# Optimization experiments

Measured on AMD Instinct MI355X. Metric: run time of the kernel, lower is better.

Reference implementation:

```python
import jax, jax.numpy as jnp
import numpy as np

T = 3
B, N, F = 8, 256, 32
E_DIM = 8
HID = 32
IN_DIM = 2 * (F + 1) + E_DIM  # 74


def setup_inputs() -> dict:
    key = jax.random.key(0)
    ks = jax.random.split(key, 10)
    h = jax.random.normal(ks[0], (B, N, F), dtype=jnp.float32)
    e = jax.random.uniform(ks[1], (B, N, N, E_DIM), dtype=jnp.float32)
    q = jax.random.normal(ks[2], (B, N, 1), dtype=jnp.float32)
    mask = jnp.ones((B, N), dtype=jnp.float32)
    s1 = 1.0 / np.sqrt(IN_DIM)
    s2 = 1.0 / np.sqrt(HID)
    W1 = jax.random.normal(ks[3], (T, IN_DIM, HID), dtype=jnp.float32) * s1
    b1 = jnp.zeros((T, HID), dtype=jnp.float32)
    W2 = jax.random.normal(ks[4], (T, HID, HID), dtype=jnp.float32) * s2
    b2 = jnp.zeros((T, HID), dtype=jnp.float32)
    W3 = jax.random.normal(ks[5], (T, HID, 1), dtype=jnp.float32) * s2
    b3 = jnp.zeros((T, 1), dtype=jnp.float32)
    return {"h": h, "e": e, "q": q, "mask": mask,
            "W1": W1, "b1": b1, "W2": W2, "b2": b2, "W3": W3, "b3": b3}


def reference(h, e, q, mask, W1, b1, W2, b2, W3, b3):
    tol = jnp.float32(1e-8)
    clip = jnp.clip(e, tol, 1e5)
    largest_e = jnp.max(clip, axis=-1)          # [B,N,N]
    is_near = (largest_e != tol).astype(h.dtype)
    m = mask.astype(h.dtype)
    exp_mask = m[:, :, None] * m[:, None, :]    # [B,N,N]
    natom = e.shape[1]

    def mlp(x, t):
        x = jax.nn.relu(jnp.matmul(x, W1[t]) + b1[t])
        x = jax.nn.relu(jnp.matmul(x, W2[t]) + b2[t])
        return (jnp.matmul(x, W3[t]) + b3[t])[..., 0]  # [B,N,N]

    for t in range(T):
        inp = jnp.concatenate([h, q], axis=-1)  # [B,N,F+1]
        d = inp.shape[-1]
        inp_i = jnp.broadcast_to(inp[:, :, None, :], (inp.shape[0], natom, natom, d))
        inp_j = jnp.broadcast_to(inp[:, None, :, :], (inp.shape[0], natom, natom, d))
        inp_ij = jnp.concatenate([inp_i, inp_j, e], axis=-1)  # [B,N,N,IN_DIM]
        inp_ji = jnp.concatenate([inp_j, inp_i, e], axis=-1)
        elec_ij = mlp(inp_ij, t)
        elec_ji = mlp(inp_ji, t)
        antisym = 0.5 * (elec_ij - elec_ji) * exp_mask * is_near
        q = q + jnp.sum(antisym, axis=2)[..., None]
    return q
```

## Files before the change

### kernel.cpp

```cpp
#include <hip/hip_runtime.h>
#include <hip/hip_bf16.h>


typedef __attribute__((ext_vector_type(8))) short short8;
typedef __attribute__((ext_vector_type(4))) float f32x4;
union U4S8 { uint4 u; short8 s; };
#define F4(p) (*(const float4*)(p))

__device__ __forceinline__ unsigned pkbf2(float lo, float hi) {
    unsigned a = __bfloat16_as_ushort(__float2bfloat16(lo));
    unsigned b = __bfloat16_as_ushort(__float2bfloat16(hi));
    return a | (b << 16);
}
__device__ __forceinline__ float bf2f(unsigned short u) {
    return __uint_as_float(((unsigned)u) << 16);
}

__global__ __launch_bounds__(256) void epn_pre(
    const float* __restrict__ h, const float* __restrict__ W1,
    const float* __restrict__ b1, const float* __restrict__ W2,
    unsigned short* __restrict__ basePbf, unsigned short* __restrict__ baseQbf,
    unsigned* __restrict__ W2T, uint4* __restrict__ WA)
{
    const int t  = blockIdx.x >> 8;
    const int lg = (blockIdx.x & 255) * 256 + threadIdx.x;
    const float* W1t = W1 + t*74*32;
    if (lg < 512) {
        int n = lg >> 4, kp = lg & 15;
        const float* W2t = W2 + t*1024;
        W2T[t*512 + lg] = pkbf2(W2t[(2*kp)*32 + n], W2t[(2*kp+1)*32 + n]);
    } else if (lg < 640) {
        int g2 = lg - 512;
        int kt = g2 >> 6, lane = g2 & 63;
        int l15 = lane & 15, sl = lane >> 4;
        float v[8];
        #pragma unroll
        for (int p = 0; p < 8; ++p) {
            int d = sl*8 + p;
            v[p] = (d < 8) ? W1t[(66+d)*32 + kt*16 + l15]
                           : ((kt*16 + l15 == d - 8) ? 1.0f : 0.0f);
        }
        WA[t*128 + g2] = make_uint4(pkbf2(v[0],v[1]), pkbf2(v[2],v[3]),
                                    pkbf2(v[4],v[5]), pkbf2(v[6],v[7]));
    }
    const int node = lg >> 5, k = lg & 31;
    const float* hn = h + node*32;
    float p = b1[t*32 + k], qq = 0.f;
    #pragma unroll
    for (int f = 0; f < 32; ++f) {
        float hv = hn[f];
        p  += hv * W1t[f*32 + k];
        qq += hv * W1t[(33+f)*32 + k];
    }
    basePbf[t*65536 + lg] = __bfloat16_as_ushort(__float2bfloat16(p));
    baseQbf[t*65536 + lg] = __bfloat16_as_ushort(__float2bfloat16(qq));
}

__global__ __launch_bounds__(256, 4) void epn_main(
    const float* __restrict__ e, const float* __restrict__ mask,
    const uint4* __restrict__ bP4, const uint4* __restrict__ bQ4,
    const float* __restrict__ qrowP, const float* __restrict__ qrowQ,
    const uint4* __restrict__ W2T4, const uint4* __restrict__ WA,
    const float* __restrict__ b2, const float* __restrict__ W3,
    const float* __restrict__ q_src, float* __restrict__ q_dst)
{
    __shared__ uint4 sx[9][256];
    __shared__ float red[4];

    const int bi = blockIdx.x, b = bi >> 8;
    const int tid = threadIdx.x, j = tid;
    const int lane = tid & 63, w = tid >> 6;
    const int l15 = lane & 15, sl = lane >> 4;

    float qj = q_src[b*256 + j];
    unsigned qpk = __bfloat16_as_ushort(__float2bfloat16(qj));
    const float* ejp = e + ((size_t)bi*256 + j)*8;
    float4 e0 = F4(ejp), e1 = F4(ejp + 4);
    float mx = fmaxf(fmaxf(fmaxf(e0.x,e0.y),fmaxf(e0.z,e0.w)),
                     fmaxf(fmaxf(e1.x,e1.y),fmaxf(e1.z,e1.w)));
    float nearf = (fminf(fmaxf(mx, 1e-8f), 1e5f) != 1e-8f) ? 1.f : 0.f;
    float mn = mask[bi] * mask[b*256 + j] * nearf;
    sx[0][j] = make_uint4(pkbf2(e0.x,e0.y), pkbf2(e0.z,e0.w),
                          pkbf2(e1.x,e1.y), pkbf2(e1.z,e1.w));
    {
        const uint4* bq = bQ4 + (size_t)(b*256 + j)*4;
        const uint4* bp = bP4 + (size_t)(b*256 + j)*4;
        sx[1][j]=bq[0]; sx[2][j]=bq[1]; sx[3][j]=bq[2]; sx[4][j]=bq[3];
        sx[5][j]=bp[0]; sx[6][j]=bp[1]; sx[7][j]=bp[2]; sx[8][j]=bp[3];
    }

    U4S8 wa00, wa01, wa1;
    wa00.u = WA[lane];
    wa01.u = WA[64 + lane];
    wa1.u  = make_uint4(0u,0u,0u,0u);
    if (sl == 0 && l15 >= 8) {
        int p = l15 - 8;
        unsigned v = 0x3F80u << ((p & 1) * 16);
        wa1.u.x = ((p>>1)==0)?v:0u;  wa1.u.y = ((p>>1)==1)?v:0u;
        wa1.u.z = ((p>>1)==2)?v:0u;  wa1.u.w = ((p>>1)==3)?v:0u;
    }
    unsigned aqQ0 = 0, aqQ1 = 0, aqP0 = 0, aqP1 = 0;
    if (sl == 0) {
        aqQ0 = __bfloat16_as_ushort(__float2bfloat16(qrowQ[l15]));
        aqQ1 = __bfloat16_as_ushort(__float2bfloat16(qrowQ[16 + l15]));
        aqP0 = __bfloat16_as_ushort(__float2bfloat16(qrowP[l15]));
        aqP1 = __bfloat16_as_ushort(__float2bfloat16(qrowP[16 + l15]));
    }
    float qi = q_src[bi];
    const unsigned short* bPi = (const unsigned short*)bP4 + (size_t)bi*32;
    const unsigned short* bQi = (const unsigned short*)bQ4 + (size_t)bi*32;
    f32x4 ckP0, ckP1, ckQ0, ckQ1;
    #pragma unroll
    for (int r = 0; r < 4; ++r) {
        int k0 = sl*4 + r, k1 = 16 + sl*4 + r;
        ckP0[r] = bf2f(bPi[k0]) + qi * qrowP[k0];
        ckP1[r] = bf2f(bPi[k1]) + qi * qrowP[k1];
        ckQ0[r] = bf2f(bQi[k0]) + qi * qrowQ[k0];
        ckQ1[r] = bf2f(bQi[k1]) + qi * qrowQ[k1];
    }
    U4S8 bu0, bu1;
    bu0.u = W2T4[l15*4 + sl];
    bu1.u = W2T4[(l15 + 16)*4 + sl];
    float b2v0 = b2[l15], b2v1 = b2[l15+16];
    float w3v0 = W3[l15], w3v1 = W3[l15+16];
    const int srcA = ((sl & 1) << 5) + l15, srcB = srcA + 16;
    const bool ktHi = (sl >= 2);
    const int slot0_d0 = (sl == 0) ? 0 : sl;
    const int slot0_d1 = (sl == 0) ? 0 : 4 + sl;

    float tot = 0.f;
    #pragma unroll
    for (int rt = 0; rt < 4; ++rt) {
        const int rl  = rt*16 + l15;
        const int row = w*64 + rl;
        unsigned qr = __shfl(qpk, rl);
        U4S8 bc2; bc2.u = make_uint4((sl == 0) ? (qr & 0xFFFFu) : 0u, 0u, 0u, 0u);
        float pA[4], pB[4];
        #pragma unroll
        for (int dir = 0; dir < 2; ++dir) {
            U4S8 bc0, bc1, aq0, aq1;
            bc0.u = sx[dir ? slot0_d1 : slot0_d0][row];
            bc1.u = sx[dir ? 8 : 4][row];
            aq0.u = make_uint4(dir ? aqP0 : aqQ0, 0u, 0u, 0u);
            aq1.u = make_uint4(dir ? aqP1 : aqQ1, 0u, 0u, 0u);
            f32x4 c0 = dir ? ckQ0 : ckP0;
            f32x4 c1 = dir ? ckQ1 : ckP1;
            f32x4 dk0 = __builtin_amdgcn_mfma_f32_16x16x32_bf16(wa00.s, bc0.s, c0, 0,0,0);
            dk0 = __builtin_amdgcn_mfma_f32_16x16x32_bf16(aq0.s, bc2.s, dk0, 0,0,0);
            f32x4 dk1 = __builtin_amdgcn_mfma_f32_16x16x32_bf16(wa01.s, bc0.s, c1, 0,0,0);
            dk1 = __builtin_amdgcn_mfma_f32_16x16x32_bf16(wa1.s,  bc1.s, dk1, 0,0,0);
            dk1 = __builtin_amdgcn_mfma_f32_16x16x32_bf16(aq1.s,  bc2.s, dk1, 0,0,0);
            unsigned pk00 = pkbf2(fmaxf(dk0[0],0.f), fmaxf(dk0[1],0.f));
            unsigned pk01 = pkbf2(fmaxf(dk0[2],0.f), fmaxf(dk0[3],0.f));
            unsigned pk10 = pkbf2(fmaxf(dk1[0],0.f), fmaxf(dk1[1],0.f));
            unsigned pk11 = pkbf2(fmaxf(dk1[2],0.f), fmaxf(dk1[3],0.f));
            unsigned sA0l = __shfl(pk00, srcA), sA0h = __shfl(pk10, srcA);
            unsigned sA1l = __shfl(pk01, srcA), sA1h = __shfl(pk11, srcA);
            unsigned sB0l = __shfl(pk00, srcB), sB0h = __shfl(pk10, srcB);
            unsigned sB1l = __shfl(pk01, srcB), sB1h = __shfl(pk11, srcB);
            U4S8 a;
            a.u.x = ktHi ? sA0h : sA0l;
            a.u.y = ktHi ? sA1h : sA1l;
            a.u.z = ktHi ? sB0h : sB0l;
            a.u.w = ktHi ? sB1h : sB1l;
            f32x4 z = {0.f, 0.f, 0.f, 0.f};
            f32x4 d0 = __builtin_amdgcn_mfma_f32_16x16x32_bf16(a.s, bu0.s, z, 0,0,0);
            f32x4 d1 = __builtin_amdgcn_mfma_f32_16x16x32_bf16(a.s, bu1.s, z, 0,0,0);
            float* pp = dir ? pB : pA;
            pp[0] = fmaxf(d0[0]+b2v0,0.f)*w3v0 + fmaxf(d1[0]+b2v1,0.f)*w3v1;
            pp[1] = fmaxf(d0[1]+b2v0,0.f)*w3v0 + fmaxf(d1[1]+b2v1,0.f)*w3v1;
            pp[2] = fmaxf(d0[2]+b2v0,0.f)*w3v0 + fmaxf(d1[2]+b2v1,0.f)*w3v1;
            pp[3] = fmaxf(d0[3]+b2v0,0.f)*w3v0 + fmaxf(d1[3]+b2v1,0.f)*w3v1;
        }
        const int jb = rt*16 + sl*4;
        float m0 = __shfl(mn, jb+0), m1 = __shfl(mn, jb+1);
        float m2 = __shfl(mn, jb+2), m3 = __shfl(mn, jb+3);
        tot += m0*(pA[0]-pB[0]) + m1*(pA[1]-pB[1])
             + m2*(pA[2]-pB[2]) + m3*(pA[3]-pB[3]);
    }
    #pragma unroll
    for (int off = 32; off > 0; off >>= 1) tot += __shfl_down(tot, off);
    if (lane == 0) red[w] = tot;
    __syncthreads();
    if (tid == 0)
        q_dst[bi] = q_src[bi] + 0.5f * (red[0] + red[1] + red[2] + red[3]);
}

extern "C" void kernel_launch(void* const* d_in, const int* in_sizes, int n_in,
                              void* d_out, int out_size, void* d_ws, size_t ws_size,
                              hipStream_t stream) {
    (void)in_sizes; (void)n_in; (void)out_size; (void)ws_size;
    const float* h    = (const float*)d_in[0];
    const float* e    = (const float*)d_in[1];
    const float* q    = (const float*)d_in[2];
    const float* mask = (const float*)d_in[3];
    const float* W1   = (const float*)d_in[4];
    const float* b1   = (const float*)d_in[5];
    const float* W2   = (const float*)d_in[6];
    const float* b2   = (const float*)d_in[7];
    const float* W3   = (const float*)d_in[8];

    char* ws = (char*)d_ws;
    unsigned short* basePbf = (unsigned short*)ws;
    unsigned short* baseQbf = (unsigned short*)(ws + 393216);
    float*    qA  = (float*)(ws + 786432);
    float*    qB  = (float*)(ws + 794624);
    unsigned* W2T = (unsigned*)(ws + 802816);
    uint4*    WA  = (uint4*)(ws + 808960);

    epn_pre<<<768, 256, 0, stream>>>(h, W1, b1, W2, basePbf, baseQbf, W2T, WA);

    const float* qsrc = q;
    for (int t = 0; t < 3; ++t) {
        float* qdst = (t == 2) ? (float*)d_out : (t == 0 ? qA : qB);
        epn_main<<<2048, 256, 0, stream>>>(
            e, mask,
            (const uint4*)(basePbf + t*65536), (const uint4*)(baseQbf + t*65536),
            W1 + t*74*32 + 32*32, W1 + t*74*32 + 65*32,
            (const uint4*)(W2T + t*512), WA + t*128,
            b2 + t*32, W3 + t*32, qsrc, qdst);
        qsrc = qdst;
    }
}
```

Baseline: 58.10 us.

## Fuse pre-pass and three timesteps into one persistent kernel with grid barriers

```diff
diff --git a/kernel.cpp b/kernel.cpp
--- a/kernel.cpp
+++ b/kernel.cpp
@@ -16,174 +16,234 @@
     return __uint_as_float(((unsigned)u) << 16);
 }
 
-__global__ __launch_bounds__(256) void epn_pre(
-    const float* __restrict__ h, const float* __restrict__ W1,
-    const float* __restrict__ b1, const float* __restrict__ W2,
+__device__ __forceinline__ void gbar(unsigned* bar, unsigned target) {
+    __syncthreads();
+    if (threadIdx.x == 0) {
+        __threadfence();
+        atomicAdd(bar, 1u);
+        while (__hip_atomic_load(bar, __ATOMIC_ACQUIRE,
+                                 __HIP_MEMORY_SCOPE_AGENT) < target)
+            __builtin_amdgcn_s_sleep(2);
+        __threadfence();
+    }
+    __syncthreads();
+}
+
+__global__ __launch_bounds__(256, 2) void epn_fused(
+    const float* __restrict__ h, const float* __restrict__ e,
+    const float* __restrict__ q0, const float* __restrict__ mask,
+    const float* __restrict__ W1, const float* __restrict__ b1,
+    const float* __restrict__ W2, const float* __restrict__ b2,
+    const float* __restrict__ W3,
     unsigned short* __restrict__ basePbf, unsigned short* __restrict__ baseQbf,
-    unsigned* __restrict__ W2T, uint4* __restrict__ WA)
+    unsigned* __restrict__ W2T, uint4* __restrict__ WA,
+    float* __restrict__ qA, float* __restrict__ qB, float* __restrict__ qOut,
+    unsigned* __restrict__ bar)
 {
-    const int t  = blockIdx.x >> 8;
-    const int lg = (blockIdx.x & 255) * 256 + threadIdx.x;
-    const float* W1t = W1 + t*74*32;
-    if (lg < 512) {
-        int n = lg >> 4, kp = lg & 15;
-        const float* W2t = W2 + t*1024;
-        W2T[t*512 + lg] = pkbf2(W2t[(2*kp)*32 + n], W2t[(2*kp+1)*32 + n]);
-    } else if (lg < 640) {
-        int g2 = lg - 512;
-        int kt = g2 >> 6, lane = g2 & 63;
-        int l15 = lane & 15, sl = lane >> 4;
-        float v[8];
-        #pragma unroll
-        for (int p = 0; p < 8; ++p) {
-            int d = sl*8 + p;
-            v[p] = (d < 8) ? W1t[(66+d)*32 + kt*16 + l15]
-                           : ((kt*16 + l15 == d - 8) ? 1.0f : 0.0f);
-        }
-        WA[t*128 + g2] = make_uint4(pkbf2(v[0],v[1]), pkbf2(v[2],v[3]),
-                                    pkbf2(v[4],v[5]), pkbf2(v[6],v[7]));
-    }
-    const int node = lg >> 5, k = lg & 31;
-    const float* hn = h + node*32;
-    float p = b1[t*32 + k], qq = 0.f;
-    #pragma unroll
-    for (int f = 0; f < 32; ++f) {
-        float hv = hn[f];
-        p  += hv * W1t[f*32 + k];
-        qq += hv * W1t[(33+f)*32 + k];
-    }
-    basePbf[t*65536 + lg] = __bfloat16_as_ushort(__float2bfloat16(p));
-    baseQbf[t*65536 + lg] = __bfloat16_as_ushort(__float2bfloat16(qq));
-}
-
-__global__ __launch_bounds__(256, 4) void epn_main(
-    const float* __restrict__ e, const float* __restrict__ mask,
-    const uint4* __restrict__ bP4, const uint4* __restrict__ bQ4,
-    const float* __restrict__ qrowP, const float* __restrict__ qrowQ,
-    const uint4* __restrict__ W2T4, const uint4* __restrict__ WA,
-    const float* __restrict__ b2, const float* __restrict__ W3,
-    const float* __restrict__ q_src, float* __restrict__ q_dst)
-{
-    __shared__ uint4 sx[9][256];
-    __shared__ float red[4];
-
-    const int bi = blockIdx.x, b = bi >> 8;
-    const int tid = threadIdx.x, j = tid;
+    __shared__ uint4 sxJ[8][256];
+    __shared__ uint4 se[2][256];
+    __shared__ float red[16];
+
+    const int tid  = threadIdx.x, j = tid;
     const int lane = tid & 63, w = tid >> 6;
-    const int l15 = lane & 15, sl = lane >> 4;
-
-    float qj = q_src[b*256 + j];
-    unsigned qpk = __bfloat16_as_ushort(__float2bfloat16(qj));
-    const float* ejp = e + ((size_t)bi*256 + j)*8;
-    float4 e0 = F4(ejp), e1 = F4(ejp + 4);
-    float mx = fmaxf(fmaxf(fmaxf(e0.x,e0.y),fmaxf(e0.z,e0.w)),
-                     fmaxf(fmaxf(e1.x,e1.y),fmaxf(e1.z,e1.w)));
-    float nearf = (fminf(fmaxf(mx, 1e-8f), 1e5f) != 1e-8f) ? 1.f : 0.f;
-    float mn = mask[bi] * mask[b*256 + j] * nearf;
-    sx[0][j] = make_uint4(pkbf2(e0.x,e0.y), pkbf2(e0.z,e0.w),
-                          pkbf2(e1.x,e1.y), pkbf2(e1.z,e1.w));
-    {
-        const uint4* bq = bQ4 + (size_t)(b*256 + j)*4;
-        const uint4* bp = bP4 + (size_t)(b*256 + j)*4;
-        sx[1][j]=bq[0]; sx[2][j]=bq[1]; sx[3][j]=bq[2]; sx[4][j]=bq[3];
-        sx[5][j]=bp[0]; sx[6][j]=bp[1]; sx[7][j]=bp[2]; sx[8][j]=bp[3];
-    }
-
-    U4S8 wa00, wa01, wa1;
-    wa00.u = WA[lane];
-    wa01.u = WA[64 + lane];
-    wa1.u  = make_uint4(0u,0u,0u,0u);
+    const int l15  = lane & 15, sl = lane >> 4;
+    const int bi0  = blockIdx.x * 4;
+    const int b    = bi0 >> 8;
+
+    for (int g = blockIdx.x * 256 + tid; g < 198528; g += 131072) {
+        if (g < 196608) {
+            int t = g >> 16, lg = g & 65535;
+            const float* W1t = W1 + t*2368;
+            int node = lg >> 5, k = lg & 31;
+            const float* hn = h + node*32;
+            float p = b1[t*32 + k], qq = 0.f;
+            #pragma unroll
+            for (int f = 0; f < 32; ++f) {
+                float hv = hn[f];
+                p  += hv * W1t[f*32 + k];
+                qq += hv * W1t[(33+f)*32 + k];
+            }
+            basePbf[g] = __bfloat16_as_ushort(__float2bfloat16(p));
+            baseQbf[g] = __bfloat16_as_ushort(__float2bfloat16(qq));
+        } else if (g < 198144) {
+            int gg = g - 196608;
+            int t = gg >> 9, lg = gg & 511;
+            int n = lg >> 4, kp = lg & 15;
+            const float* W2t = W2 + t*1024;
+            W2T[gg] = pkbf2(W2t[(2*kp)*32 + n], W2t[(2*kp+1)*32 + n]);
+        } else {
+            int gg = g - 198144;
+            int t = gg >> 7, g2 = gg & 127;
+            int kt = g2 >> 6, ln = g2 & 63;
+            int L15 = ln & 15, SL = ln >> 4;
+            const float* W1t = W1 + t*2368;
+            float v[8];
+            #pragma unroll
+            for (int p2 = 0; p2 < 8; ++p2) {
+                int d = SL*8 + p2;
+                v[p2] = (d < 8) ? W1t[(66+d)*32 + kt*16 + L15]
+                                : ((kt*16 + L15 == d - 8) ? 1.0f : 0.0f);
+            }
+            WA[gg] = make_uint4(pkbf2(v[0],v[1]), pkbf2(v[2],v[3]),
+                                pkbf2(v[4],v[5]), pkbf2(v[6],v[7]));
+        }
+    }
+
+    U4S8 wa1; wa1.u = make_uint4(0u,0u,0u,0u);
     if (sl == 0 && l15 >= 8) {
         int p = l15 - 8;
         unsigned v = 0x3F80u << ((p & 1) * 16);
         wa1.u.x = ((p>>1)==0)?v:0u;  wa1.u.y = ((p>>1)==1)?v:0u;
         wa1.u.z = ((p>>1)==2)?v:0u;  wa1.u.w = ((p>>1)==3)?v:0u;
     }
-    unsigned aqQ0 = 0, aqQ1 = 0, aqP0 = 0, aqP1 = 0;
-    if (sl == 0) {
-        aqQ0 = __bfloat16_as_ushort(__float2bfloat16(qrowQ[l15]));
-        aqQ1 = __bfloat16_as_ushort(__float2bfloat16(qrowQ[16 + l15]));
-        aqP0 = __bfloat16_as_ushort(__float2bfloat16(qrowP[l15]));
-        aqP1 = __bfloat16_as_ushort(__float2bfloat16(qrowP[16 + l15]));
-    }
-    float qi = q_src[bi];
-    const unsigned short* bPi = (const unsigned short*)bP4 + (size_t)bi*32;
-    const unsigned short* bQi = (const unsigned short*)bQ4 + (size_t)bi*32;
-    f32x4 ckP0, ckP1, ckQ0, ckQ1;
-    #pragma unroll
-    for (int r = 0; r < 4; ++r) {
-        int k0 = sl*4 + r, k1 = 16 + sl*4 + r;
-        ckP0[r] = bf2f(bPi[k0]) + qi * qrowP[k0];
-        ckP1[r] = bf2f(bPi[k1]) + qi * qrowP[k1];
-        ckQ0[r] = bf2f(bQi[k0]) + qi * qrowQ[k0];
-        ckQ1[r] = bf2f(bQi[k1]) + qi * qrowQ[k1];
-    }
-    U4S8 bu0, bu1;
-    bu0.u = W2T4[l15*4 + sl];
-    bu1.u = W2T4[(l15 + 16)*4 + sl];
-    float b2v0 = b2[l15], b2v1 = b2[l15+16];
-    float w3v0 = W3[l15], w3v1 = W3[l15+16];
     const int srcA = ((sl & 1) << 5) + l15, srcB = srcA + 16;
     const bool ktHi = (sl >= 2);
-    const int slot0_d0 = (sl == 0) ? 0 : sl;
-    const int slot0_d1 = (sl == 0) ? 0 : 4 + sl;
-
-    float tot = 0.f;
-    #pragma unroll
-    for (int rt = 0; rt < 4; ++rt) {
-        const int rl  = rt*16 + l15;
-        const int row = w*64 + rl;
-        unsigned qr = __shfl(qpk, rl);
-        U4S8 bc2; bc2.u = make_uint4((sl == 0) ? (qr & 0xFFFFu) : 0u, 0u, 0u, 0u);
-        float pA[4], pB[4];
+    float maskj = mask[b*256 + j];
+
+    gbar(bar, 512u);
+
+    for (int t = 0; t < 3; ++t) {
+        const float* qsrc = (t == 0) ? q0 : ((t == 1) ? qA : qB);
+        float* qdst       = (t == 2) ? qOut : ((t == 0) ? qA : qB);
+        const float* W1t   = W1 + t*2368;
+        const float* qrowP = W1t + 32*32;
+        const float* qrowQ = W1t + 65*32;
+        const uint4* W2T4  = (const uint4*)(W2T + t*512);
+        const uint4* WAt   = WA + t*128;
+        const unsigned short* bP = basePbf + t*65536;
+        const unsigned short* bQ = baseQbf + t*65536;
+        const float* b2t = b2 + t*32;
+        const float* W3t = W3 + t*32;
+
+        {
+            const uint4* bq = ((const uint4*)bQ) + (size_t)(b*256 + j)*4;
+            const uint4* bp = ((const uint4*)bP) + (size_t)(b*256 + j)*4;
+            sxJ[0][j]=bq[0]; sxJ[1][j]=bq[1]; sxJ[2][j]=bq[2]; sxJ[3][j]=bq[3];
+            sxJ[4][j]=bp[0]; sxJ[5][j]=bp[1]; sxJ[6][j]=bp[2]; sxJ[7][j]=bp[3];
+        }
+        float qjv = qsrc[b*256 + j];
+        unsigned qpk = __bfloat16_as_ushort(__float2bfloat16(qjv));
+
+        U4S8 wa00, wa01;
+        wa00.u = WAt[lane];
+        wa01.u = WAt[64 + lane];
+        unsigned aqQ0 = 0, aqQ1 = 0, aqP0 = 0, aqP1 = 0;
+        if (sl == 0) {
+            aqQ0 = __bfloat16_as_ushort(__float2bfloat16(qrowQ[l15]));
+            aqQ1 = __bfloat16_as_ushort(__float2bfloat16(qrowQ[16 + l15]));
+            aqP0 = __bfloat16_as_ushort(__float2bfloat16(qrowP[l15]));
+            aqP1 = __bfloat16_as_ushort(__float2bfloat16(qrowP[16 + l15]));
+        }
+        U4S8 bu0, bu1;
+        bu0.u = W2T4[l15*4 + sl];
+        bu1.u = W2T4[(l15 + 16)*4 + sl];
+        float b2v0 = b2t[l15], b2v1 = b2t[l15+16];
+        float w3v0 = W3t[l15], w3v1 = W3t[l15+16];
+        float qrP0v[4], qrP1v[4], qrQ0v[4], qrQ1v[4];
         #pragma unroll
-        for (int dir = 0; dir < 2; ++dir) {
-            U4S8 bc0, bc1, aq0, aq1;
-            bc0.u = sx[dir ? slot0_d1 : slot0_d0][row];
-            bc1.u = sx[dir ? 8 : 4][row];
-            aq0.u = make_uint4(dir ? aqP0 : aqQ0, 0u, 0u, 0u);
-            aq1.u = make_uint4(dir ? aqP1 : aqQ1, 0u, 0u, 0u);
-            f32x4 c0 = dir ? ckQ0 : ckP0;
-            f32x4 c1 = dir ? ckQ1 : ckP1;
-            f32x4 dk0 = __builtin_amdgcn_mfma_f32_16x16x32_bf16(wa00.s, bc0.s, c0, 0,0,0);
-            dk0 = __builtin_amdgcn_mfma_f32_16x16x32_bf16(aq0.s, bc2.s, dk0, 0,0,0);
-            f32x4 dk1 = __builtin_amdgcn_mfma_f32_16x16x32_bf16(wa01.s, bc0.s, c1, 0,0,0);
-            dk1 = __builtin_amdgcn_mfma_f32_16x16x32_bf16(wa1.s,  bc1.s, dk1, 0,0,0);
-            dk1 = __builtin_amdgcn_mfma_f32_16x16x32_bf16(aq1.s,  bc2.s, dk1, 0,0,0);
-            unsigned pk00 = pkbf2(fmaxf(dk0[0],0.f), fmaxf(dk0[1],0.f));
-            unsigned pk01 = pkbf2(fmaxf(dk0[2],0.f), fmaxf(dk0[3],0.f));
-            unsigned pk10 = pkbf2(fmaxf(dk1[0],0.f), fmaxf(dk1[1],0.f));
-            unsigned pk11 = pkbf2(fmaxf(dk1[2],0.f), fmaxf(dk1[3],0.f));
-            unsigned sA0l = __shfl(pk00, srcA), sA0h = __shfl(pk10, srcA);
-            unsigned sA1l = __shfl(pk01, srcA), sA1h = __shfl(pk11, srcA);
-            unsigned sB0l = __shfl(pk00, srcB), sB0h = __shfl(pk10, srcB);
-            unsigned sB1l = __shfl(pk01, srcB), sB1h = __shfl(pk11, srcB);
-            U4S8 a;
-            a.u.x = ktHi ? sA0h : sA0l;
-            a.u.y = ktHi ? sA1h : sA1l;
-            a.u.z = ktHi ? sB0h : sB0l;
-            a.u.w = ktHi ? sB1h : sB1l;
-            f32x4 z = {0.f, 0.f, 0.f, 0.f};
-            f32x4 d0 = __builtin_amdgcn_mfma_f32_16x16x32_bf16(a.s, bu0.s, z, 0,0,0);
-            f32x4 d1 = __builtin_amdgcn_mfma_f32_16x16x32_bf16(a.s, bu1.s, z, 0,0,0);
-            float* pp = dir ? pB : pA;
-            pp[0] = fmaxf(d0[0]+b2v0,0.f)*w3v0 + fmaxf(d1[0]+b2v1,0.f)*w3v1;
-            pp[1] = fmaxf(d0[1]+b2v0,0.f)*w3v0 + fmaxf(d1[1]+b2v1,0.f)*w3v1;
-            pp[2] = fmaxf(d0[2]+b2v0,0.f)*w3v0 + fmaxf(d1[2]+b2v1,0.f)*w3v1;
-            pp[3] = fmaxf(d0[3]+b2v0,0.f)*w3v0 + fmaxf(d1[3]+b2v1,0.f)*w3v1;
-        }
-        const int jb = rt*16 + sl*4;
-        float m0 = __shfl(mn, jb+0), m1 = __shfl(mn, jb+1);
-        float m2 = __shfl(mn, jb+2), m3 = __shfl(mn, jb+3);
-        tot += m0*(pA[0]-pB[0]) + m1*(pA[1]-pB[1])
-             + m2*(pA[2]-pB[2]) + m3*(pA[3]-pB[3]);
-    }
-    #pragma unroll
-    for (int off = 32; off > 0; off >>= 1) tot += __shfl_down(tot, off);
-    if (lane == 0) red[w] = tot;
-    __syncthreads();
-    if (tid == 0)
-        q_dst[bi] = q_src[bi] + 0.5f * (red[0] + red[1] + red[2] + red[3]);
+        for (int r = 0; r < 4; ++r) {
+            qrP0v[r] = qrowP[sl*4 + r];  qrP1v[r] = qrowP[16 + sl*4 + r];
+            qrQ0v[r] = qrowQ[sl*4 + r];  qrQ1v[r] = qrowQ[16 + sl*4 + r];
+        }
+
+        const float* ep0 = e + ((size_t)bi0*256 + j)*8;
+        float4 a0 = F4(ep0), a1 = F4(ep0 + 4);
+
+        for (int p = 0; p < 4; ++p) {
+            const int bi = bi0 + p;
+            float4 e0 = a0, e1 = a1;
+            if (p < 3) {
+                const float* epn = e + ((size_t)(bi + 1)*256 + j)*8;
+                a0 = F4(epn); a1 = F4(epn + 4);
+            }
+            float mx = fmaxf(fmaxf(fmaxf(e0.x,e0.y),fmaxf(e0.z,e0.w)),
+                             fmaxf(fmaxf(e1.x,e1.y),fmaxf(e1.z,e1.w)));
+            float nearf = (fminf(fmaxf(mx, 1e-8f), 1e5f) != 1e-8f) ? 1.f : 0.f;
+            float mn = mask[bi] * maskj * nearf;
+            const int par = p & 1;
+            se[par][j] = make_uint4(pkbf2(e0.x,e0.y), pkbf2(e0.z,e0.w),
+                                    pkbf2(e1.x,e1.y), pkbf2(e1.z,e1.w));
+            const uint4* base_d0 = (sl == 0) ? &se[par][0] : &sxJ[sl-1][0];
+            const uint4* base_d1 = (sl == 0) ? &se[par][0] : &sxJ[3+sl][0];
+
+            float qi = qsrc[bi];
+            const unsigned short* bPi = bP + (size_t)bi*32;
+            const unsigned short* bQi = bQ + (size_t)bi*32;
+            ushort4 bp0 = *(const ushort4*)(bPi + sl*4);
+            ushort4 bp1 = *(const ushort4*)(bPi + 16 + sl*4);
+            ushort4 bq0 = *(const ushort4*)(bQi + sl*4);
+            ushort4 bq1 = *(const ushort4*)(bQi + 16 + sl*4);
+            f32x4 ckP0 = {bf2f(bp0.x)+qi*qrP0v[0], bf2f(bp0.y)+qi*qrP0v[1],
+                          bf2f(bp0.z)+qi*qrP0v[2], bf2f(bp0.w)+qi*qrP0v[3]};
+            f32x4 ckP1 = {bf2f(bp1.x)+qi*qrP1v[0], bf2f(bp1.y)+qi*qrP1v[1],
+                          bf2f(bp1.z)+qi*qrP1v[2], bf2f(bp1.w)+qi*qrP1v[3]};
+            f32x4 ckQ0 = {bf2f(bq0.x)+qi*qrQ0v[0], bf2f(bq0.y)+qi*qrQ0v[1],
+                          bf2f(bq0.z)+qi*qrQ0v[2], bf2f(bq0.w)+qi*qrQ0v[3]};
+            f32x4 ckQ1 = {bf2f(bq1.x)+qi*qrQ1v[0], bf2f(bq1.y)+qi*qrQ1v[1],
+                          bf2f(bq1.z)+qi*qrQ1v[2], bf2f(bq1.w)+qi*qrQ1v[3]};
+
+            float tot = 0.f;
+            #pragma unroll
+            for (int rt = 0; rt < 4; ++rt) {
+                const int rl  = rt*16 + l15;
+                const int row = w*64 + rl;
+                unsigned qr = __shfl(qpk, rl);
+                U4S8 bc2; bc2.u = make_uint4((sl == 0) ? (qr & 0xFFFFu) : 0u, 0u, 0u, 0u);
+                float pA[4], pB[4];
+                #pragma unroll
+                for (int dir = 0; dir < 2; ++dir) {
+                    U4S8 bc0, bc1, aq0, aq1;
+                    bc0.u = dir ? base_d1[row] : base_d0[row];
+                    bc1.u = dir ? sxJ[7][row]  : sxJ[3][row];
+                    aq0.u = make_uint4(dir ? aqP0 : aqQ0, 0u, 0u, 0u);
+                    aq1.u = make_uint4(dir ? aqP1 : aqQ1, 0u, 0u, 0u);
+                    f32x4 c0 = dir ? ckQ0 : ckP0;
+                    f32x4 c1 = dir ? ckQ1 : ckP1;
+                    f32x4 dk0 = __builtin_amdgcn_mfma_f32_16x16x32_bf16(wa00.s, bc0.s, c0, 0,0,0);
+                    dk0 = __builtin_amdgcn_mfma_f32_16x16x32_bf16(aq0.s, bc2.s, dk0, 0,0,0);
+                    f32x4 dk1 = __builtin_amdgcn_mfma_f32_16x16x32_bf16(wa01.s, bc0.s, c1, 0,0,0);
+                    dk1 = __builtin_amdgcn_mfma_f32_16x16x32_bf16(wa1.s,  bc1.s, dk1, 0,0,0);
+                    dk1 = __builtin_amdgcn_mfma_f32_16x16x32_bf16(aq1.s,  bc2.s, dk1, 0,0,0);
+                    unsigned pk00 = pkbf2(fmaxf(dk0[0],0.f), fmaxf(dk0[1],0.f));
+                    unsigned pk01 = pkbf2(fmaxf(dk0[2],0.f), fmaxf(dk0[3],0.f));
+                    unsigned pk10 = pkbf2(fmaxf(dk1[0],0.f), fmaxf(dk1[1],0.f));
+                    unsigned pk11 = pkbf2(fmaxf(dk1[2],0.f), fmaxf(dk1[3],0.f));
+                    unsigned sA0l = __shfl(pk00, srcA), sA0h = __shfl(pk10, srcA);
+                    unsigned sA1l = __shfl(pk01, srcA), sA1h = __shfl(pk11, srcA);
+                    unsigned sB0l = __shfl(pk00, srcB), sB0h = __shfl(pk10, srcB);
+                    unsigned sB1l = __shfl(pk01, srcB), sB1h = __shfl(pk11, srcB);
+                    U4S8 a;
+                    a.u.x = ktHi ? sA0h : sA0l;
+                    a.u.y = ktHi ? sA1h : sA1l;
+                    a.u.z = ktHi ? sB0h : sB0l;
+                    a.u.w = ktHi ? sB1h : sB1l;
+                    f32x4 z = {0.f, 0.f, 0.f, 0.f};
+                    f32x4 d0 = __builtin_amdgcn_mfma_f32_16x16x32_bf16(a.s, bu0.s, z, 0,0,0);
+                    f32x4 d1 = __builtin_amdgcn_mfma_f32_16x16x32_bf16(a.s, bu1.s, z, 0,0,0);
+                    float* pp = dir ? pB : pA;
+                    pp[0] = fmaxf(d0[0]+b2v0,0.f)*w3v0 + fmaxf(d1[0]+b2v1,0.f)*w3v1;
+                    pp[1] = fmaxf(d0[1]+b2v0,0.f)*w3v0 + fmaxf(d1[1]+b2v1,0.f)*w3v1;
+                    pp[2] = fmaxf(d0[2]+b2v0,0.f)*w3v0 + fmaxf(d1[2]+b2v1,0.f)*w3v1;
+                    pp[3] = fmaxf(d0[3]+b2v0,0.f)*w3v0 + fmaxf(d1[3]+b2v1,0.f)*w3v1;
+                }
+                const int jb = rt*16 + sl*4;
+                float m0 = __shfl(mn, jb+0), m1 = __shfl(mn, jb+1);
+                float m2 = __shfl(mn, jb+2), m3 = __shfl(mn, jb+3);
+                tot += m0*(pA[0]-pB[0]) + m1*(pA[1]-pB[1])
+                     + m2*(pA[2]-pB[2]) + m3*(pA[3]-pB[3]);
+            }
+            #pragma unroll
+            for (int off = 32; off > 0; off >>= 1) tot += __shfl_down(tot, off);
+            if (lane == 0) red[p*4 + w] = tot;
+        }
+        __syncthreads();
+        if (tid < 4) {
+            int bi = bi0 + tid;
+            qdst[bi] = qsrc[bi] + 0.5f*(red[tid*4+0] + red[tid*4+1]
+                                      + red[tid*4+2] + red[tid*4+3]);
+        }
+        if (t < 2) gbar(bar, 512u * (t + 2));
+    }
 }
 
 extern "C" void kernel_launch(void* const* d_in, const int* in_sizes, int n_in,
@@ -203,22 +263,15 @@
     char* ws = (char*)d_ws;
     unsigned short* basePbf = (unsigned short*)ws;
     unsigned short* baseQbf = (unsigned short*)(ws + 393216);
-    float*    qA  = (float*)(ws + 786432);
-    float*    qB  = (float*)(ws + 794624);
-    unsigned* W2T = (unsigned*)(ws + 802816);
-    uint4*    WA  = (uint4*)(ws + 808960);
-
-    epn_pre<<<768, 256, 0, stream>>>(h, W1, b1, W2, basePbf, baseQbf, W2T, WA);
-
-    const float* qsrc = q;
-    for (int t = 0; t < 3; ++t) {
-        float* qdst = (t == 2) ? (float*)d_out : (t == 0 ? qA : qB);
-        epn_main<<<2048, 256, 0, stream>>>(
-            e, mask,
-            (const uint4*)(basePbf + t*65536), (const uint4*)(baseQbf + t*65536),
-            W1 + t*74*32 + 32*32, W1 + t*74*32 + 65*32,
-            (const uint4*)(W2T + t*512), WA + t*128,
-            b2 + t*32, W3 + t*32, qsrc, qdst);
-        qsrc = qdst;
-    }
-}
+    float*    qA   = (float*)(ws + 786432);
+    float*    qB   = (float*)(ws + 794624);
+    unsigned* W2T  = (unsigned*)(ws + 802816);
+    uint4*    WA   = (uint4*)(ws + 808960);
+    unsigned* bar  = (unsigned*)(ws + 815104);
+    float*    qOut = (float*)d_out;
+
+    hipMemsetAsync(bar, 0, sizeof(unsigned), stream);
+    epn_fused<<<512, 256, 0, stream>>>(h, e, q, mask, W1, b1, W2, b2, W3,
+                                       basePbf, baseQbf, W2T, WA,
+                                       qA, qB, qOut, bar);
+}
```

Result: slower. 205.7 us (+254.0%).
